# Kernel optimization log

Measured on AMD Instinct MI355X. Metric: run time of the kernel, lower is better.

## Reference

```python
import jax, jax.numpy as jnp
import numpy as np

IMG_W, IMG_H = 960.0, 512.0  # image_size from cfg


def setup_inputs() -> dict:
    B, N, J = 4, 5, 15
    Hh, Wh = 128, 240
    rng = np.random.default_rng(0)
    heatmaps = jnp.asarray(rng.random((N, B, J, Hh, Wh)).astype(np.float32))
    # rotations near identity (orthonormalized, det=+1)
    A = np.eye(3, dtype=np.float32) + 0.05 * rng.normal(size=(B, N, 3, 3)).astype(np.float32)
    Q = np.linalg.qr(A)[0]
    det = np.linalg.det(Q)
    Q[..., :, 0] = Q[..., :, 0] * det[..., None]
    R = jnp.asarray(Q.astype(np.float32))
    # cameras ~5m behind the volume so cam-z > 0 everywhere
    T = jnp.asarray((np.array([0.0, 0.0, -5000.0], np.float32) + 100.0 * rng.normal(size=(B, N, 3))).astype(np.float32))
    f = jnp.asarray((1000.0 + 20.0 * rng.normal(size=(B, N, 2))).astype(np.float32))
    c = jnp.asarray(np.tile(np.array([IMG_W / 2, IMG_H / 2], np.float32), (B, N, 1)))
    trans = jnp.asarray(np.tile(np.array([[1.0, 0.0, 0.0], [0.0, 1.0, 0.0]], np.float32), (B, N, 1, 1)))
    wh = jnp.asarray(np.tile(np.array([IMG_W, IMG_H], np.float32), (B, N, 1)))  # width,height = center*2
    gc = np.stack([rng.uniform(-500, 500, B), rng.uniform(-500, 500, B), np.full(B, 1000.0)], axis=1).astype(np.float32)
    grid_center = jnp.asarray(gc)
    return dict(heatmaps=heatmaps, R=R, T=T, f=f, c=c, trans=trans, wh=wh,
                grid_center=grid_center, gs_x=8000, gs_y=8000, gs_z=2000,
                cb_x=80, cb_y=80, cb_z=20)


def _bilinear(img, g):
    # img [J,H,W], g [P,2] in normalized coords; align_corners=True, zero padding
    Jn, H, W = img.shape
    x = (g[:, 0] + 1.0) * 0.5 * (W - 1)
    y = (g[:, 1] + 1.0) * 0.5 * (H - 1)
    x0 = jnp.floor(x)
    y0 = jnp.floor(y)
    wx = x - x0
    wy = y - y0

    def gather(xi, yi):
        valid = ((xi >= 0) & (xi <= W - 1) & (yi >= 0) & (yi <= H - 1)).astype(img.dtype)
        xc = jnp.clip(xi, 0, W - 1).astype(jnp.int32)
        yc = jnp.clip(yi, 0, H - 1).astype(jnp.int32)
        return img[:, yc, xc] * valid  # [J,P]

    return (gather(x0, y0) * (1 - wx) * (1 - wy) + gather(x0 + 1, y0) * wx * (1 - wy)
            + gather(x0, y0 + 1) * (1 - wx) * wy + gather(x0 + 1, y0 + 1) * wx * wy)


def _forward(heatmaps, R, T, f, c, trans, wh, grid_center, gs_x, gs_y, gs_z, cb_x, cb_y, cb_z):
    N, B, J, Hh, Wh = heatmaps.shape
    P = cb_x * cb_y * cb_z
    # compute_grid: world-space voxel centers per batch
    gx = jnp.linspace(-gs_x / 2, gs_x / 2, cb_x)
    gy = jnp.linspace(-gs_y / 2, gs_y / 2, cb_y)
    gz = jnp.linspace(-gs_z / 2, gs_z / 2, cb_z)
    mx, my, mz = jnp.meshgrid(gx, gy, gz, indexing='ij')
    base = jnp.stack([mx.ravel(), my.ravel(), mz.ravel()], axis=-1).astype(jnp.float32)  # [P,3]
    grids = base[None] + grid_center[:, None, :]                                         # [B,P,3]
    # world_to_pixel (pinhole): cam = R (X - T); pixel = f*cam_xy/cam_z + c
    diff = grids[:, None, :, :] - T[:, :, None, :]              # [B,N,P,3]
    cam = jnp.einsum('bnij,bnpj->bnpi', R, diff)                # [B,N,P,3]
    xy = cam[..., :2] / cam[..., 2:3] * f[:, :, None, :] + c[:, :, None, :]  # [B,N,P,2]
    width = wh[..., 0][:, :, None]
    height = wh[..., 1][:, :, None]
    bound = ((xy[..., 0] >= 0) & (xy[..., 1] >= 0) &
             (xy[..., 0] < width) & (xy[..., 1] < height)).astype(jnp.float32)  # [B,N,P]
    maxwh = jnp.maximum(width, height)[..., None]
    xy = jnp.clip(xy, -1.0, maxwh)
    # affine transform to model-input frame, then rescale to heatmap frame
    xy = jnp.einsum('bnij,bnpj->bnpi', trans[..., :2], xy) + trans[..., 2][:, :, None, :]
    xy = xy * jnp.array([Wh, Hh], jnp.float32) / jnp.array([IMG_W, IMG_H], jnp.float32)
    sg = jnp.clip(xy / jnp.array([Wh - 1, Hh - 1], jnp.float32) * 2.0 - 1.0, -1.1, 1.1)  # [B,N,P,2]
    imgs = jnp.transpose(heatmaps, (1, 0, 2, 3, 4)).reshape(B * N, J, Hh, Wh)
    samples = jax.vmap(_bilinear)(imgs, sg.reshape(B * N, P, 2))   # [B*N,J,P]
    cubes = jnp.transpose(samples.reshape(B, N, J, P), (0, 2, 3, 1))  # [B,J,P,N]
    wmask = jnp.transpose(bound, (0, 2, 1))[:, None]                  # [B,1,P,N]
    fused = jnp.sum(cubes * wmask, axis=-1) / (jnp.sum(wmask, axis=-1) + 1e-6)  # [B,J,P]
    fused = jnp.where(jnp.isnan(fused), 0.0, fused)
    fused = jnp.clip(fused, 0.0, 1.0).reshape(B, J, cb_x, cb_y, cb_z)
    return fused, grids


def reference(heatmaps, R, T, f, c, trans, wh, grid_center, gs_x, gs_y, gs_z, cb_x, cb_y, cb_z):
    return _forward(heatmaps, R, T, f, c, trans, wh, grid_center,
                    gs_x, gs_y, gs_z, cb_x, cb_y, cb_z)
```

## Files before the change

kernel.cpp:

```cpp
#include <hip/hip_runtime.h>

#define BB   4
#define NN   5
#define JJ   15
#define HHH  128
#define WHH  240
#define CBX  80
#define CBY  80
#define CBZ  20
#define PP   (CBX*CBY*CBZ)
#define HW   (HHH*WHH)
#define IMGW 960.0f
#define IMGH 512.0f

__global__ __launch_bounds__(256) void project_kernel(
    const float* __restrict__ hm,
    const float* __restrict__ Rm,
    const float* __restrict__ Tv,
    const float* __restrict__ fv,
    const float* __restrict__ cv,
    const float* __restrict__ trans,
    const float* __restrict__ whv,
    const float* __restrict__ gcv,
    float* __restrict__ out)
{
    int t = blockIdx.x * blockDim.x + threadIdx.x;
    if (t >= BB * PP) return;
    int b = t / PP;
    int p = t - b * PP;
    int ix  = p / (CBY * CBZ);
    int rem = p - ix * (CBY * CBZ);
    int iy  = rem / CBZ;
    int iz  = rem - iy * CBZ;

    const float stx = 8000.0f / (CBX - 1);
    const float sty = 8000.0f / (CBY - 1);
    const float stz = 2000.0f / (CBZ - 1);
    float gx = -4000.0f + (float)ix * stx + gcv[b * 3 + 0];
    float gy = -4000.0f + (float)iy * sty + gcv[b * 3 + 1];
    float gz = -1000.0f + (float)iz * stz + gcv[b * 3 + 2];

    {
        float* grids_out = out + (size_t)BB * JJ * PP;
        size_t gb = (size_t)(b * PP + p) * 3;
        grids_out[gb + 0] = gx;
        grids_out[gb + 1] = gy;
        grids_out[gb + 2] = gz;
    }

    float wl0[NN], wr0[NN], wl1[NN], wr1[NN];
    int   r0[NN], r1[NN];
    float bnd[NN];
    float sumb = 0.0f;

    #pragma unroll
    for (int n = 0; n < NN; ++n) {
        int bn = b * NN + n;
        const float* R = Rm + bn * 9;
        float dx = gx - Tv[bn * 3 + 0];
        float dy = gy - Tv[bn * 3 + 1];
        float dz = gz - Tv[bn * 3 + 2];
        float cx = R[0] * dx + R[1] * dy + R[2] * dz;
        float cy = R[3] * dx + R[4] * dy + R[5] * dz;
        float cz = R[6] * dx + R[7] * dy + R[8] * dz;
        float inv = 1.0f / cz;
        float px = cx * inv * fv[bn * 2 + 0] + cv[bn * 2 + 0];
        float py = cy * inv * fv[bn * 2 + 1] + cv[bn * 2 + 1];
        float w = whv[bn * 2 + 0], h = whv[bn * 2 + 1];
        float bound = (px >= 0.0f && py >= 0.0f && px < w && py < h) ? 1.0f : 0.0f;
        float mwh = fmaxf(w, h);
        px = fminf(fmaxf(px, -1.0f), mwh);
        py = fminf(fmaxf(py, -1.0f), mwh);
        const float* tr = trans + bn * 6;
        float tx = tr[0] * px + tr[1] * py + tr[2];
        float ty = tr[3] * px + tr[4] * py + tr[5];
        tx *= (float)WHH / IMGW;
        ty *= (float)HHH / IMGH;
        float sgx = tx / (float)(WHH - 1) * 2.0f - 1.0f;
        float sgy = ty / (float)(HHH - 1) * 2.0f - 1.0f;
        sgx = fminf(fmaxf(sgx, -1.1f), 1.1f);
        sgy = fminf(fmaxf(sgy, -1.1f), 1.1f);
        float xx = (sgx + 1.0f) * 0.5f * (float)(WHH - 1);
        float yy = (sgy + 1.0f) * 0.5f * (float)(HHH - 1);
        float x0f = floorf(xx), y0f = floorf(yy);
        float wx = xx - x0f, wy = yy - y0f;
        int x0 = (int)x0f, y0 = (int)y0f;

        float axl, axr;
        if (x0 < 0) {
            float vx1 = (x0 + 1 >= 0) ? 1.0f : 0.0f;
            axl = wx * vx1;
            axr = 0.0f;
        } else if (x0 >= WHH - 1) {
            float vx0 = (x0 <= WHH - 1) ? 1.0f : 0.0f;
            axl = 0.0f;
            axr = (1.0f - wx) * vx0;
        } else {
            axl = 1.0f - wx;
            axr = wx;
        }
        int xb = min(max(x0, 0), WHH - 2);

        float vy0 = (y0 >= 0 && y0 <= HHH - 1) ? 1.0f : 0.0f;
        float vy1 = (y0 + 1 >= 0 && y0 + 1 <= HHH - 1) ? 1.0f : 0.0f;
        int yc0 = min(max(y0, 0), HHH - 1);
        int yc1 = min(max(y0 + 1, 0), HHH - 1);
        float ay0 = (1.0f - wy) * vy0 * bound;
        float ay1 = wy * vy1 * bound;

        wl0[n] = axl * ay0;  wr0[n] = axr * ay0;
        wl1[n] = axl * ay1;  wr1[n] = axr * ay1;
        r0[n] = yc0 * WHH + xb;
        r1[n] = yc1 * WHH + xb;
        bnd[n] = bound;
        sumb += bound;
    }

    float acc[JJ];
    #pragma unroll
    for (int j = 0; j < JJ; ++j) acc[j] = 0.0f;

    #pragma unroll
    for (int n = 0; n < NN; ++n) {
        if (bnd[n] != 0.0f) {
            const float* base = hm + (size_t)((n * BB + b) * JJ) * HW;
            float c00 = wl0[n], c01 = wr0[n], c10 = wl1[n], c11 = wr1[n];
            int o0 = r0[n], o1 = r1[n];
            #pragma unroll
            for (int j = 0; j < JJ; ++j) {
                const float* pj = base + j * HW;
                float2 e = *reinterpret_cast<const float2*>(pj + o0);
                float2 f2 = *reinterpret_cast<const float2*>(pj + o1);
                acc[j] += c00 * e.x + c01 * e.y + c10 * f2.x + c11 * f2.y;
            }
        }
    }

    float denom = 1.0f / (sumb + 1e-6f);
    size_t outb = (size_t)b * JJ * PP + p;
    #pragma unroll
    for (int j = 0; j < JJ; ++j) {
        float v = acc[j] * denom;
        v = fminf(fmaxf(v, 0.0f), 1.0f);
        out[outb + (size_t)j * PP] = v;
    }
}

extern "C" void kernel_launch(void* const* d_in, const int* in_sizes, int n_in,
                              void* d_out, int out_size, void* d_ws, size_t ws_size,
                              hipStream_t stream) {
    const float* hm    = (const float*)d_in[0];
    const float* Rm    = (const float*)d_in[1];
    const float* Tv    = (const float*)d_in[2];
    const float* fv    = (const float*)d_in[3];
    const float* cv    = (const float*)d_in[4];
    const float* trans = (const float*)d_in[5];
    const float* whv   = (const float*)d_in[6];
    const float* gcv   = (const float*)d_in[7];
    float* out = (float*)d_out;

    int total = BB * PP;
    int block = 256;
    int grid  = (total + block - 1) / block;
    project_kernel<<<grid, block, 0, stream>>>(hm, Rm, Tv, fv, cv, trans, whv, gcv, out);
}
```

Measured before the change: 173.1 us.

## Transpose heatmaps to pixel-major layout with joints/views contiguous for vector gathers

Adds a pre-pass kernel that rewrites the heatmaps into a workspace laid out as [B][y][x][view*16+joint], padding joints to 16. The projection kernel then fetches each bilinear corner as four float4 loads per view instead of 15 scattered float2 loads spread across joint planes. This targets the gather cost of the main kernel, which touches many separate cache lines. In exchange it adds an extra kernel that reads the full heatmap tensor and writes a padded copy of it every call.

```diff
diff --git a/kernel.cpp b/kernel.cpp
--- a/kernel.cpp
+++ b/kernel.cpp
@@ -12,9 +12,34 @@
 #define HW   (HHH*WHH)
 #define IMGW 960.0f
 #define IMGH 512.0f
+#define NJP  80
+#define XT   60
+
+__global__ __launch_bounds__(256) void transpose_kernel(
+    const float* __restrict__ hm, float* __restrict__ ws)
+{
+    int bid = blockIdx.x;
+    int xt = bid & 3;
+    int y  = (bid >> 2) & (HHH - 1);
+    int b  = bid >> 9;
+    int x0 = xt * XT;
+    size_t wsb = ((size_t)(b * HHH + y) * WHH + x0) * NJP;
+    const int total = XT * NJP;
+    for (int off = threadIdx.x; off < total; off += 256) {
+        int x = off / NJP;
+        int q = off - x * NJP;
+        int n = q >> 4;
+        int j = q & 15;
+        float v = 0.0f;
+        if (j < JJ) {
+            v = hm[((size_t)(n * BB + b) * JJ + j) * HW + y * WHH + x0 + x];
+        }
+        ws[wsb + off] = v;
+    }
+}
 
 __global__ __launch_bounds__(256) void project_kernel(
-    const float* __restrict__ hm,
+    const float* __restrict__ ws,
     const float* __restrict__ Rm,
     const float* __restrict__ Tv,
     const float* __restrict__ fv,
@@ -120,18 +145,30 @@
     #pragma unroll
     for (int j = 0; j < JJ; ++j) acc[j] = 0.0f;
 
+    size_t base_b = (size_t)b * HHH * WHH * NJP;
+
     #pragma unroll
     for (int n = 0; n < NN; ++n) {
         if (bnd[n] != 0.0f) {
-            const float* base = hm + (size_t)((n * BB + b) * JJ) * HW;
+            size_t a0 = base_b + (size_t)r0[n] * NJP + n * 16;
+            size_t a1 = base_b + (size_t)r1[n] * NJP + n * 16;
+            const float4* p00 = reinterpret_cast<const float4*>(ws + a0);
+            const float4* p01 = reinterpret_cast<const float4*>(ws + a0 + NJP);
+            const float4* p10 = reinterpret_cast<const float4*>(ws + a1);
+            const float4* p11 = reinterpret_cast<const float4*>(ws + a1 + NJP);
+            float f00[16], f01[16], f10[16], f11[16];
+            #pragma unroll
+            for (int k = 0; k < 4; ++k) {
+                float4 v0 = p00[k], v1 = p01[k], v2 = p10[k], v3 = p11[k];
+                f00[4*k] = v0.x; f00[4*k+1] = v0.y; f00[4*k+2] = v0.z; f00[4*k+3] = v0.w;
+                f01[4*k] = v1.x; f01[4*k+1] = v1.y; f01[4*k+2] = v1.z; f01[4*k+3] = v1.w;
+                f10[4*k] = v2.x; f10[4*k+1] = v2.y; f10[4*k+2] = v2.z; f10[4*k+3] = v2.w;
+                f11[4*k] = v3.x; f11[4*k+1] = v3.y; f11[4*k+2] = v3.z; f11[4*k+3] = v3.w;
+            }
             float c00 = wl0[n], c01 = wr0[n], c10 = wl1[n], c11 = wr1[n];
-            int o0 = r0[n], o1 = r1[n];
             #pragma unroll
             for (int j = 0; j < JJ; ++j) {
-                const float* pj = base + j * HW;
-                float2 e = *reinterpret_cast<const float2*>(pj + o0);
-                float2 f2 = *reinterpret_cast<const float2*>(pj + o1);
-                acc[j] += c00 * e.x + c01 * e.y + c10 * f2.x + c11 * f2.y;
+                acc[j] += c00 * f00[j] + c01 * f01[j] + c10 * f10[j] + c11 * f11[j];
             }
         }
     }
@@ -158,9 +195,12 @@
     const float* whv   = (const float*)d_in[6];
     const float* gcv   = (const float*)d_in[7];
     float* out = (float*)d_out;
+    float* ws  = (float*)d_ws;
+
+    transpose_kernel<<<BB * HHH * 4, 256, 0, stream>>>(hm, ws);
 
     int total = BB * PP;
     int block = 256;
     int grid  = (total + block - 1) / block;
-    project_kernel<<<grid, block, 0, stream>>>(hm, Rm, Tv, fv, cv, trans, whv, gcv, out);
+    project_kernel<<<grid, block, 0, stream>>>(ws, Rm, Tv, fv, cv, trans, whv, gcv, out);
 }
```

Result: slower. 184.4 us (+6.5%).

## Repack heatmaps into fp16 joint-interleaved pairs for single-line bilinear gathers

Applied to the files above, without the earlier changes.

Adds a pre-pass kernel that transposes heatmaps into a workspace where each (b, y, n, x) holds all joints contiguously, each as an fp16 pair of horizontally adjacent texels. The projection kernel then fetches one 64-byte record per row tap with vector loads instead of 15 scattered float2 loads per camera, which should cut memory transactions and cache-line traffic. In exchange it adds a pack pass over the full heatmap tensor every call and reduces sample precision to fp16.

```diff
diff --git a/kernel.cpp b/kernel.cpp
--- a/kernel.cpp
+++ b/kernel.cpp
@@ -1,4 +1,5 @@
 #include <hip/hip_runtime.h>
+#include <hip/hip_fp16.h>
 
 #define BB   4
 #define NN   5
@@ -12,9 +13,43 @@
 #define HW   (HHH*WHH)
 #define IMGW 960.0f
 #define IMGH 512.0f
+#define RECU 16
+
+
+__global__ __launch_bounds__(256) void pack_kernel(
+    const float* __restrict__ hm, unsigned int* __restrict__ ws)
+{
+    __shared__ float rows[JJ][WHH + 1];
+    int bid = blockIdx.x;
+    int n = bid % NN;
+    int y = (bid / NN) % HHH;
+    int b = bid / (NN * HHH);
+
+    const float* src = hm + ((size_t)(n * BB + b) * JJ) * HW + y * WHH;
+    for (int idx = threadIdx.x; idx < JJ * (WHH + 1); idx += 256) {
+        int j = idx / (WHH + 1);
+        int x = idx - j * (WHH + 1);
+        int xs = min(x, WHH - 1);
+        rows[j][x] = src[j * HW + xs];
+    }
+    __syncthreads();
+
+    unsigned int* dst = ws + (size_t)((b * HHH + y) * NN + n) * WHH * RECU;
+    for (int idx = threadIdx.x; idx < WHH * RECU; idx += 256) {
+        int x = idx >> 4;
+        int u = idx & 15;
+        unsigned int val = 0u;
+        if (u < JJ) {
+            __half2 h = __halves2half2(__float2half_rn(rows[u][x]),
+                                       __float2half_rn(rows[u][x + 1]));
+            val = *reinterpret_cast<unsigned int*>(&h);
+        }
+        dst[idx] = val;
+    }
+}
 
 __global__ __launch_bounds__(256) void project_kernel(
-    const float* __restrict__ hm,
+    const unsigned int* __restrict__ ws,
     const float* __restrict__ Rm,
     const float* __restrict__ Tv,
     const float* __restrict__ fv,
@@ -48,7 +83,7 @@
         grids_out[gb + 2] = gz;
     }
 
-    float wl0[NN], wr0[NN], wl1[NN], wr1[NN];
+    float cl0[NN], cr0[NN], cl1[NN], cr1[NN];
     int   r0[NN], r1[NN];
     float bnd[NN];
     float sumb = 0.0f;
@@ -86,20 +121,14 @@
         float wx = xx - x0f, wy = yy - y0f;
         int x0 = (int)x0f, y0 = (int)y0f;
 
-        float axl, axr;
+        float axl, axr; int xb;
         if (x0 < 0) {
-            float vx1 = (x0 + 1 >= 0) ? 1.0f : 0.0f;
-            axl = wx * vx1;
-            axr = 0.0f;
+            axl = (x0 == -1) ? wx : 0.0f; axr = 0.0f; xb = 0;
         } else if (x0 >= WHH - 1) {
-            float vx0 = (x0 <= WHH - 1) ? 1.0f : 0.0f;
-            axl = 0.0f;
-            axr = (1.0f - wx) * vx0;
+            axl = (x0 == WHH - 1) ? (1.0f - wx) : 0.0f; axr = 0.0f; xb = WHH - 1;
         } else {
-            axl = 1.0f - wx;
-            axr = wx;
+            axl = 1.0f - wx; axr = wx; xb = x0;
         }
-        int xb = min(max(x0, 0), WHH - 2);
 
         float vy0 = (y0 >= 0 && y0 <= HHH - 1) ? 1.0f : 0.0f;
         float vy1 = (y0 + 1 >= 0 && y0 + 1 <= HHH - 1) ? 1.0f : 0.0f;
@@ -108,10 +137,10 @@
         float ay0 = (1.0f - wy) * vy0 * bound;
         float ay1 = wy * vy1 * bound;
 
-        wl0[n] = axl * ay0;  wr0[n] = axr * ay0;
-        wl1[n] = axl * ay1;  wr1[n] = axr * ay1;
-        r0[n] = yc0 * WHH + xb;
-        r1[n] = yc1 * WHH + xb;
+        cl0[n] = axl * ay0;  cr0[n] = axr * ay0;
+        cl1[n] = axl * ay1;  cr1[n] = axr * ay1;
+        r0[n] = ((((b * HHH + yc0) * NN + n) * WHH) + xb) * RECU;
+        r1[n] = ((((b * HHH + yc1) * NN + n) * WHH) + xb) * RECU;
         bnd[n] = bound;
         sumb += bound;
     }
@@ -123,15 +152,22 @@
     #pragma unroll
     for (int n = 0; n < NN; ++n) {
         if (bnd[n] != 0.0f) {
-            const float* base = hm + (size_t)((n * BB + b) * JJ) * HW;
-            float c00 = wl0[n], c01 = wr0[n], c10 = wl1[n], c11 = wr1[n];
-            int o0 = r0[n], o1 = r1[n];
+            const uint4* q0 = reinterpret_cast<const uint4*>(ws + r0[n]);
+            const uint4* q1 = reinterpret_cast<const uint4*>(ws + r1[n]);
+            uint4 a0 = q0[0], a1 = q0[1], a2 = q0[2], a3 = q0[3];
+            uint4 b0 = q1[0], b1 = q1[1], b2 = q1[2], b3 = q1[3];
+            float c0l = cl0[n], c0r = cr0[n], c1l = cl1[n], c1r = cr1[n];
+            unsigned int s0[16] = {a0.x,a0.y,a0.z,a0.w, a1.x,a1.y,a1.z,a1.w,
+                                   a2.x,a2.y,a2.z,a2.w, a3.x,a3.y,a3.z,a3.w};
+            unsigned int s1[16] = {b0.x,b0.y,b0.z,b0.w, b1.x,b1.y,b1.z,b1.w,
+                                   b2.x,b2.y,b2.z,b2.w, b3.x,b3.y,b3.z,b3.w};
             #pragma unroll
             for (int j = 0; j < JJ; ++j) {
-                const float* pj = base + j * HW;
-                float2 e = *reinterpret_cast<const float2*>(pj + o0);
-                float2 f2 = *reinterpret_cast<const float2*>(pj + o1);
-                acc[j] += c00 * e.x + c01 * e.y + c10 * f2.x + c11 * f2.y;
+                __half2 h0 = *reinterpret_cast<__half2*>(&s0[j]);
+                __half2 h1 = *reinterpret_cast<__half2*>(&s1[j]);
+                float2 f0 = __half22float2(h0);
+                float2 f1 = __half22float2(h1);
+                acc[j] += c0l * f0.x + c0r * f0.y + c1l * f1.x + c1r * f1.y;
             }
         }
     }
@@ -158,9 +194,12 @@
     const float* whv   = (const float*)d_in[6];
     const float* gcv   = (const float*)d_in[7];
     float* out = (float*)d_out;
+    unsigned int* ws = (unsigned int*)d_ws;
+
+    pack_kernel<<<BB * HHH * NN, 256, 0, stream>>>(hm, ws);
 
     int total = BB * PP;
     int block = 256;
     int grid  = (total + block - 1) / block;
-    project_kernel<<<grid, block, 0, stream>>>(hm, Rm, Tv, fv, cv, trans, whv, gcv, out);
+    project_kernel<<<grid, block, 0, stream>>>(ws, Rm, Tv, fv, cv, trans, whv, gcv, out);
 }
```

Result: faster. 153.5 us (-11.4%).
